# Performance work log

Measured on AMD Instinct MI355X. Metric: run time of the kernel, lower is better.

Reference implementation:

```python
import jax, jax.numpy as jnp
import numpy as np

D_MODEL = 1024
N_HEADS = 16
D_K = D_MODEL // N_HEADS
B, S = 2, 2048


def setup_inputs() -> dict:
    key = jax.random.key(0)
    ks = jax.random.split(key, 5)
    sc = 1.0 / np.sqrt(D_MODEL)
    return {
        "x": jax.random.normal(ks[0], (B, S, D_MODEL), dtype=jnp.float32),
        "W_qkv": jax.random.normal(ks[1], (D_MODEL, 3 * D_MODEL), dtype=jnp.float32) * sc,
        "b_qkv": jnp.zeros((3 * D_MODEL,), dtype=jnp.float32),
        "W_out": jax.random.normal(ks[2], (D_MODEL, D_MODEL), dtype=jnp.float32) * sc,
        "b_out": jnp.zeros((D_MODEL,), dtype=jnp.float32),
    }


def reference(x, W_qkv, b_qkv, W_out, b_out):
    Bb, Ss, _ = x.shape
    qkv = x @ W_qkv + b_qkv                     # [B,S,3*D]
    qkv = qkv.reshape(Bb, Ss, 3, N_HEADS, D_K)
    qkv = jnp.transpose(qkv, (2, 0, 3, 1, 4))   # [3,B,H,S,Dk]
    q, k, v = qkv[0], qkv[1], qkv[2]
    scale = jnp.asarray(np.sqrt(D_K), dtype=x.dtype)
    attn = jnp.einsum('bhsd,bhtd->bhst', q, k) / scale  # [B,H,S,S]
    attn = jax.nn.softmax(attn, axis=-1)
    out = jnp.einsum('bhst,bhtd->bhsd', attn, v)        # [B,H,S,Dk]
    out = jnp.transpose(out, (0, 2, 1, 3)).reshape(Bb, Ss, D_MODEL)
    return out @ W_out + b_out
```

## Files before the change

### kernel.cpp

```cpp
#include <hip/hip_runtime.h>

typedef __bf16 bf16x8 __attribute__((ext_vector_type(8)));
typedef __bf16 bf16x4 __attribute__((ext_vector_type(4)));
typedef float f32x4 __attribute__((ext_vector_type(4)));
typedef unsigned short u16;
typedef unsigned int u32;

__device__ __forceinline__ u16 f2bu(float f) {
  __bf16 h = (__bf16)f;
  return __builtin_bit_cast(u16, h);
}

__device__ __forceinline__ void gld16(const u16* g, const __bf16* lds) {
  __builtin_amdgcn_global_load_lds(
      (const __attribute__((address_space(1))) u32*)(uintptr_t)g,
      (__attribute__((address_space(3))) u32*)(u32)(uintptr_t)lds, 16, 0, 0);
}

__device__ __forceinline__ void tr_tile(const float* __restrict__ in, u16* __restrict__ out,
                                        int R, int C, int bx, int by, int tid) {
  __shared__ u16 t[64][65];
  int tx = tid & 63, ty = tid >> 6;
  int r0 = by * 64, c0 = bx * 64;
  for (int i = 0; i < 16; ++i)
    t[ty + i * 4][tx] = f2bu(in[(size_t)(r0 + ty + i * 4) * C + c0 + tx]);
  __syncthreads();
  for (int i = 0; i < 16; ++i)
    out[(size_t)(c0 + ty + i * 4) * R + r0 + tx] = t[tx][ty + i * 4];
}

__global__ __launch_bounds__(256) void prep(const float* __restrict__ Wqkv,
                                            u16* __restrict__ Wqkv_t,
                                            const float* __restrict__ Wout,
                                            u16* __restrict__ Wout_t,
                                            const float* __restrict__ x,
                                            u16* __restrict__ xb) {
  int id = blockIdx.x, tid = threadIdx.x;
  if (id < 768) {
    tr_tile(Wqkv, Wqkv_t, 1024, 3072, id % 48, id / 48, tid);
  } else if (id < 1024) {
    int id2 = id - 768;
    tr_tile(Wout, Wout_t, 1024, 1024, id2 % 16, id2 / 16, tid);
  } else {
    size_t i = ((size_t)(id - 1024) * 256 + tid) * 8;
    f32x4 a0 = *(const f32x4*)(x + i);
    f32x4 a1 = *(const f32x4*)(x + i + 4);
    bf16x8 v;
    for (int j = 0; j < 4; ++j) { v[j] = (__bf16)a0[j]; v[j + 4] = (__bf16)a1[j]; }
    *(bf16x8*)(xb + i) = v;
  }
}

__global__ __launch_bounds__(256) void transpose_v(const u16* __restrict__ V,
                                                   u16* __restrict__ Vt) {
  constexpr int S = 2048;
  __shared__ u16 t[64][65];
  int bh = blockIdx.y, s0 = blockIdx.x * 64;
  const u16* in = V + (size_t)bh * S * 64;
  u16* out = Vt + (size_t)bh * 64 * S;
  int tx = threadIdx.x & 63, ty = threadIdx.x >> 6;
  for (int i = 0; i < 16; ++i)
    t[ty + i * 4][tx] = in[(size_t)(s0 + ty + i * 4) * 64 + tx];
  __syncthreads();
  for (int i = 0; i < 16; ++i)
    out[(size_t)(ty + i * 4) * S + s0 + tx] = t[tx][ty + i * 4];
}

template <int MODE, int TM, int TN, int MT, int NT, int XM, int XN>
__global__ __launch_bounds__(256) void gemm_bt(const u16* __restrict__ A,
                                               const u16* __restrict__ Bt,
                                               const float* __restrict__ bias,
                                               void* __restrict__ O0v,
                                               u16* __restrict__ O1,
                                               u16* __restrict__ O2,
                                               int M, int N, int K) {
  constexpr int NI = TM / 32;
  constexpr int NJ = TN / 32;
  constexpr int AE = TM * 32;
  constexpr int BE = TN * 32;
  __shared__ __bf16 smem[2 * (AE + BE)];

  int tid = threadIdx.x;
  int w = tid >> 6, lane = tid & 63, quad = lane >> 4, l16 = lane & 15;
  int wr = w >> 1, wc = w & 1;

  int id = blockIdx.x;
  int xcd = id & 7, s0i = id >> 3;
  int mg = xcd % (MT / XM), ng = xcd / (MT / XM);
  int sm = s0i % XM, sn = s0i / XM;
  int m0 = (mg * XM + sm) * TM, n0 = (ng * XN + sn) * TN;

  int srow = w * 16 + (lane >> 2);
  int sch = (lane & 3) ^ ((lane >> 3) & 3);
  const u16* Ag = A + (size_t)(m0 + srow) * K + sch * 8;
  const u16* Bg = Bt + (size_t)(n0 + srow) * K + sch * 8;

  int swl = (quad ^ ((l16 >> 1) & 3)) << 3;

  f32x4 acc[NI][NJ] = {};

#define GLD_STEP(c, kk)                                                          \
  {                                                                              \
    for (int p = 0; p < TM / 64; ++p)                                            \
      gld16(Ag + (size_t)p * 64 * K + (kk), smem + (c) * (AE + BE) + w * 512 + p * 2048); \
    for (int p = 0; p < TN / 64; ++p)                                            \
      gld16(Bg + (size_t)p * 64 * K + (kk), smem + (c) * (AE + BE) + AE + w * 512 + p * 2048); \
  }

  GLD_STEP(0, 0);
  int NS = K / 32;
  for (int s = 0; s < NS; ++s) {
    int cur = s & 1;
    __syncthreads();
    if (s + 1 < NS) GLD_STEP(1 - cur, (s + 1) * 32);
    const __bf16* Asub = smem + cur * (AE + BE);
    const __bf16* Bsub = Asub + AE;
    bf16x8 af[NI], bfr[NJ];
    for (int i = 0; i < NI; ++i)
      af[i] = *(const bf16x8*)(Asub + (wr * (TM / 2) + i * 16 + l16) * 32 + swl);
    for (int j = 0; j < NJ; ++j)
      bfr[j] = *(const bf16x8*)(Bsub + (wc * (TN / 2) + j * 16 + l16) * 32 + swl);
    for (int i = 0; i < NI; ++i)
      for (int j = 0; j < NJ; ++j)
        acc[i][j] = __builtin_amdgcn_mfma_f32_16x16x32_bf16(af[i], bfr[j], acc[i][j], 0, 0, 0);
  }
#undef GLD_STEP

  if (MODE == 0) {
    float* O0 = (float*)O0v;
    for (int j = 0; j < NJ; ++j) {
      int n = n0 + wc * (TN / 2) + j * 16 + l16;
      float bv = bias[n];
      for (int i = 0; i < NI; ++i) {
        int mb = m0 + wr * (TM / 2) + i * 16 + quad * 4;
        for (int r = 0; r < 4; ++r)
          O0[(size_t)(mb + r) * N + n] = acc[i][j][r] + bv;
      }
    }
  } else {
    u16* O0 = (u16*)O0v;
    for (int j = 0; j < NJ; ++j) {
      int n = n0 + wc * (TN / 2) + j * 16 + l16;
      int which = n >> 10, rem = n & 1023, h = rem >> 6, d = rem & 63;
      float bv = bias[n];
      for (int i = 0; i < NI; ++i) {
        for (int r = 0; r < 4; ++r) {
          int m = m0 + wr * (TM / 2) + i * 16 + quad * 4 + r;
          int b = m >> 11, s = m & 2047;
          size_t o = (((size_t)(b * 16 + h)) * 2048 + s) * 64 + d;
          u16 val = f2bu(acc[i][j][r] + bv);
          if (which == 0) O0[o] = val;
          else if (which == 1) O1[o] = val;
          else O2[o] = val;
        }
      }
    }
  }
}

__global__ __launch_bounds__(256, 2) void flash_attn(const u16* __restrict__ Q,
                                                     const u16* __restrict__ K,
                                                     const u16* __restrict__ Vt,
                                                     u16* __restrict__ AO) {
  constexpr int S = 2048;
  __shared__ __bf16 Ks[2][64 * 64];
  __shared__ __bf16 Vs[2][64 * 64];
  __shared__ __bf16 Ps[4][32 * 64];

  int bh = blockIdx.x, qbase = blockIdx.y * 128;
  int tid = threadIdx.x, w = tid >> 6, lane = tid & 63, quad = lane >> 4, l16 = lane & 15;

  const u16* Qh = Q + (size_t)bh * S * 64;
  const u16* Kh = K + (size_t)bh * S * 64;
  const u16* Vh = Vt + (size_t)bh * 64 * S;

  int qrowA = qbase + w * 32 + l16;
  int qrowB = qrowA + 16;
  bf16x8 qf0a = *(const bf16x8*)(Qh + (size_t)qrowA * 64 + quad * 8);
  bf16x8 qf1a = *(const bf16x8*)(Qh + (size_t)qrowA * 64 + 32 + quad * 8);
  bf16x8 qf0b = *(const bf16x8*)(Qh + (size_t)qrowB * 64 + quad * 8);
  bf16x8 qf1b = *(const bf16x8*)(Qh + (size_t)qrowB * 64 + 32 + quad * 8);

  int r0s = tid >> 3, b0s = tid & 7;
  int r1s = r0s + 32;
  int ko0 = r0s * 64 + ((b0s ^ (r0s & 7)) << 3);
  int ko1 = r1s * 64 + ((b0s ^ (r1s & 7)) << 3);

  bf16x8 kr0, kr1, vr0, vr1;
#define LOAD_TILE(tb)                                                   \
  {                                                                     \
    kr0 = *(const bf16x8*)(Kh + (size_t)((tb) + r0s) * 64 + b0s * 8);   \
    kr1 = *(const bf16x8*)(Kh + (size_t)((tb) + r1s) * 64 + b0s * 8);   \
    vr0 = *(const bf16x8*)(Vh + (size_t)r0s * S + (tb) + b0s * 8);      \
    vr1 = *(const bf16x8*)(Vh + (size_t)r1s * S + (tb) + b0s * 8);      \
  }
#define STORE_TILE(c)                                                   \
  {                                                                     \
    *(bf16x8*)(&Ks[c][ko0]) = kr0;                                      \
    *(bf16x8*)(&Ks[c][ko1]) = kr1;                                      \
    *(bf16x8*)(&Vs[c][ko0]) = vr0;                                      \
    *(bf16x8*)(&Vs[c][ko1]) = vr1;                                      \
  }

  LOAD_TILE(0);
  STORE_TILE(0);
  LOAD_TILE(64);
  __syncthreads();

  constexpr float C1 = 0.125f * 1.44269504f;
  constexpr float C0 = -12.0f * 1.44269504f;

  float lA = 0.f, lB = 0.f;
  f32x4 oA[4] = {};
  f32x4 oB[4] = {};
  int xr = l16 & 7;
  int pw_baseA = l16 * 64 + (quad & 1) * 4;
  int pw_baseB = (l16 + 16) * 64 + (quad & 1) * 4;
  int pw_blk = quad >> 1;

  for (int it = 0; it < S / 64; ++it) {
    int c = it & 1;
    if (it + 1 < S / 64) STORE_TILE(1 - c);
    if (it + 2 < S / 64) LOAD_TILE((it + 2) * 64);

    for (int nt = 0; nt < 4; ++nt) {
      const __bf16* kb = &Ks[c][(nt * 16 + l16) * 64];
      bf16x8 kf0 = *(const bf16x8*)(kb + ((quad ^ xr) << 3));
      bf16x8 kf1 = *(const bf16x8*)(kb + (((quad + 4) ^ xr) << 3));
      f32x4 ca = {0.f, 0.f, 0.f, 0.f};
      f32x4 cb = {0.f, 0.f, 0.f, 0.f};
      ca = __builtin_amdgcn_mfma_f32_16x16x32_bf16(kf0, qf0a, ca, 0, 0, 0);
      cb = __builtin_amdgcn_mfma_f32_16x16x32_bf16(kf0, qf0b, cb, 0, 0, 0);
      ca = __builtin_amdgcn_mfma_f32_16x16x32_bf16(kf1, qf1a, ca, 0, 0, 0);
      cb = __builtin_amdgcn_mfma_f32_16x16x32_bf16(kf1, qf1b, cb, 0, 0, 0);
      bf16x4 pka, pkb;
      for (int r = 0; r < 4; ++r) {
        float pa = __builtin_amdgcn_exp2f(fmaf(ca[r], C1, C0));
        float pb = __builtin_amdgcn_exp2f(fmaf(cb[r], C1, C0));
        lA += pa;
        lB += pb;
        pka[r] = (__bf16)pa;
        pkb[r] = (__bf16)pb;
      }
      int pc = (((nt * 2 + pw_blk) ^ xr) << 3);
      *(bf16x4*)(&Ps[w][pw_baseA + pc]) = pka;
      *(bf16x4*)(&Ps[w][pw_baseB + pc]) = pkb;
    }

    bf16x8 pf0a = *(const bf16x8*)(&Ps[w][l16 * 64 + ((quad ^ xr) << 3)]);
    bf16x8 pf1a = *(const bf16x8*)(&Ps[w][l16 * 64 + (((quad + 4) ^ xr) << 3)]);
    bf16x8 pf0b = *(const bf16x8*)(&Ps[w][(l16 + 16) * 64 + ((quad ^ xr) << 3)]);
    bf16x8 pf1b = *(const bf16x8*)(&Ps[w][(l16 + 16) * 64 + (((quad + 4) ^ xr) << 3)]);
    for (int dt = 0; dt < 4; ++dt) {
      const __bf16* vb = &Vs[c][(dt * 16 + l16) * 64];
      bf16x8 v0 = *(const bf16x8*)(vb + ((quad ^ xr) << 3));
      bf16x8 v1 = *(const bf16x8*)(vb + (((quad + 4) ^ xr) << 3));
      oA[dt] = __builtin_amdgcn_mfma_f32_16x16x32_bf16(pf0a, v0, oA[dt], 0, 0, 0);
      oB[dt] = __builtin_amdgcn_mfma_f32_16x16x32_bf16(pf0b, v0, oB[dt], 0, 0, 0);
      oA[dt] = __builtin_amdgcn_mfma_f32_16x16x32_bf16(pf1a, v1, oA[dt], 0, 0, 0);
      oB[dt] = __builtin_amdgcn_mfma_f32_16x16x32_bf16(pf1b, v1, oB[dt], 0, 0, 0);
    }
    __syncthreads();
  }
#undef LOAD_TILE
#undef STORE_TILE

  lA += __shfl_xor(lA, 16);
  lA += __shfl_xor(lA, 32);
  lB += __shfl_xor(lB, 16);
  lB += __shfl_xor(lB, 32);
  float linvA[4], linvB[4];
  for (int r = 0; r < 4; ++r) {
    linvA[r] = 1.f / __shfl(lA, quad * 4 + r);
    linvB[r] = 1.f / __shfl(lB, quad * 4 + r);
  }

  int b = bh >> 4, h = bh & 15;
  for (int dt = 0; dt < 4; ++dt)
    for (int r = 0; r < 4; ++r) {
      int sA = qbase + w * 32 + quad * 4 + r;
      int sB = sA + 16;
      int d = dt * 16 + l16;
      AO[(((size_t)b * 2048 + sA) * 16 + h) * 64 + d] = f2bu(oA[dt][r] * linvA[r]);
      AO[(((size_t)b * 2048 + sB) * 16 + h) * 64 + d] = f2bu(oB[dt][r] * linvB[r]);
    }
}

extern "C" void kernel_launch(void* const* d_in, const int* in_sizes, int n_in,
                              void* d_out, int out_size, void* d_ws, size_t ws_size,
                              hipStream_t stream) {
  const float* x    = (const float*)d_in[0];
  const float* Wqkv = (const float*)d_in[1];
  const float* bqkv = (const float*)d_in[2];
  const float* Wout = (const float*)d_in[3];
  const float* bout = (const float*)d_in[4];
  float* out = (float*)d_out;

  u16* ws = (u16*)d_ws;
  size_t off = 0;
  u16* Wqkv_t = ws + off; off += (size_t)3072 * 1024;
  u16* Wout_t = ws + off; off += (size_t)1024 * 1024;
  u16* xb     = ws + off; off += (size_t)4096 * 1024;
  u16* Qb     = ws + off; off += (size_t)32 * 2048 * 64;
  u16* Kb     = ws + off; off += (size_t)32 * 2048 * 64;
  u16* Vb     = ws + off; off += (size_t)32 * 2048 * 64;
  u16* Vtb    = ws + off; off += (size_t)32 * 2048 * 64;
  u16* AO     = xb;

  prep<<<dim3(3072), 256, 0, stream>>>(Wqkv, Wqkv_t, Wout, Wout_t, x, xb);
  gemm_bt<1, 128, 128, 32, 24, 8, 12><<<dim3(768), 256, 0, stream>>>(
      xb, Wqkv_t, bqkv, (void*)Qb, Kb, Vb, 4096, 3072, 1024);
  transpose_v<<<dim3(32, 32), 256, 0, stream>>>(Vb, Vtb);
  flash_attn<<<dim3(32, 16), 256, 0, stream>>>(Qb, Kb, Vtb, AO);
  gemm_bt<0, 128, 64, 32, 16, 8, 8><<<dim3(512), 256, 0, stream>>>(
      AO, Wout_t, bout, (void*)out, nullptr, nullptr, 4096, 1024, 1024);
}
```

Before: 180.0 us.

## Fuse V transpose into QKV GEMM epilogue and load K/V directly into registers

The QKV GEMM epilogue now writes V already transposed, using vectorized 4-element stores, so the separate transpose kernel and its V buffer are gone. Flash attention drops LDS staging and __syncthreads for K and V. Each lane loads its MFMA fragments straight from global memory, with K prefetched one tile ahead in registers. The grid is remapped so heads are grouped per XCD for L2 locality, and MFMA sections get raised wave priority. The trade-off is more register pressure and redundant global loads across waves in exchange for removing LDS traffic, barriers and one kernel launch.

```diff
diff --git a/kernel.cpp b/kernel.cpp
--- a/kernel.cpp
+++ b/kernel.cpp
@@ -4,6 +4,7 @@
 typedef __bf16 bf16x4 __attribute__((ext_vector_type(4)));
 typedef float f32x4 __attribute__((ext_vector_type(4)));
 typedef unsigned short u16;
+typedef unsigned short u16x4 __attribute__((ext_vector_type(4)));
 typedef unsigned int u32;
 
 __device__ __forceinline__ u16 f2bu(float f) {
@@ -51,21 +52,6 @@
   }
 }
 
-__global__ __launch_bounds__(256) void transpose_v(const u16* __restrict__ V,
-                                                   u16* __restrict__ Vt) {
-  constexpr int S = 2048;
-  __shared__ u16 t[64][65];
-  int bh = blockIdx.y, s0 = blockIdx.x * 64;
-  const u16* in = V + (size_t)bh * S * 64;
-  u16* out = Vt + (size_t)bh * 64 * S;
-  int tx = threadIdx.x & 63, ty = threadIdx.x >> 6;
-  for (int i = 0; i < 16; ++i)
-    t[ty + i * 4][tx] = in[(size_t)(s0 + ty + i * 4) * 64 + tx];
-  __syncthreads();
-  for (int i = 0; i < 16; ++i)
-    out[(size_t)(ty + i * 4) * S + s0 + tx] = t[tx][ty + i * 4];
-}
-
 template <int MODE, int TM, int TN, int MT, int NT, int XM, int XN>
 __global__ __launch_bounds__(256) void gemm_bt(const u16* __restrict__ A,
                                                const u16* __restrict__ Bt,
@@ -144,14 +130,16 @@
       int which = n >> 10, rem = n & 1023, h = rem >> 6, d = rem & 63;
       float bv = bias[n];
       for (int i = 0; i < NI; ++i) {
-        for (int r = 0; r < 4; ++r) {
-          int m = m0 + wr * (TM / 2) + i * 16 + quad * 4 + r;
-          int b = m >> 11, s = m & 2047;
-          size_t o = (((size_t)(b * 16 + h)) * 2048 + s) * 64 + d;
-          u16 val = f2bu(acc[i][j][r] + bv);
-          if (which == 0) O0[o] = val;
-          else if (which == 1) O1[o] = val;
-          else O2[o] = val;
+        int m = m0 + wr * (TM / 2) + i * 16 + quad * 4;
+        int b = m >> 11, s = m & 2047;
+        if (which == 2) {
+          u16x4 val;
+          for (int r = 0; r < 4; ++r) val[r] = f2bu(acc[i][j][r] + bv);
+          *(u16x4*)(O2 + (((size_t)(b * 16 + h)) * 64 + d) * 2048 + s) = val;
+        } else {
+          u16* Od = which ? O1 : O0;
+          for (int r = 0; r < 4; ++r)
+            Od[(((size_t)(b * 16 + h)) * 2048 + (s + r)) * 64 + d] = f2bu(acc[i][j][r] + bv);
         }
       }
     }
@@ -163,11 +151,14 @@
                                                      const u16* __restrict__ Vt,
                                                      u16* __restrict__ AO) {
   constexpr int S = 2048;
-  __shared__ __bf16 Ks[2][64 * 64];
-  __shared__ __bf16 Vs[2][64 * 64];
+  constexpr int NITER = S / 64;
   __shared__ __bf16 Ps[4][32 * 64];
 
-  int bh = blockIdx.x, qbase = blockIdx.y * 128;
+  int id = blockIdx.x;
+  int xcd = id & 7, kk = id >> 3;
+  int bh = xcd * 4 + (kk & 3);
+  int qbase = (kk >> 2) * 128;
+
   int tid = threadIdx.x, w = tid >> 6, lane = tid & 63, quad = lane >> 4, l16 = lane & 15;
 
   const u16* Qh = Q + (size_t)bh * S * 64;
@@ -181,31 +172,8 @@
   bf16x8 qf0b = *(const bf16x8*)(Qh + (size_t)qrowB * 64 + quad * 8);
   bf16x8 qf1b = *(const bf16x8*)(Qh + (size_t)qrowB * 64 + 32 + quad * 8);
 
-  int r0s = tid >> 3, b0s = tid & 7;
-  int r1s = r0s + 32;
-  int ko0 = r0s * 64 + ((b0s ^ (r0s & 7)) << 3);
-  int ko1 = r1s * 64 + ((b0s ^ (r1s & 7)) << 3);
-
-  bf16x8 kr0, kr1, vr0, vr1;
-#define LOAD_TILE(tb)                                                   \
-  {                                                                     \
-    kr0 = *(const bf16x8*)(Kh + (size_t)((tb) + r0s) * 64 + b0s * 8);   \
-    kr1 = *(const bf16x8*)(Kh + (size_t)((tb) + r1s) * 64 + b0s * 8);   \
-    vr0 = *(const bf16x8*)(Vh + (size_t)r0s * S + (tb) + b0s * 8);      \
-    vr1 = *(const bf16x8*)(Vh + (size_t)r1s * S + (tb) + b0s * 8);      \
-  }
-#define STORE_TILE(c)                                                   \
-  {                                                                     \
-    *(bf16x8*)(&Ks[c][ko0]) = kr0;                                      \
-    *(bf16x8*)(&Ks[c][ko1]) = kr1;                                      \
-    *(bf16x8*)(&Vs[c][ko0]) = vr0;                                      \
-    *(bf16x8*)(&Vs[c][ko1]) = vr1;                                      \
-  }
-
-  LOAD_TILE(0);
-  STORE_TILE(0);
-  LOAD_TILE(64);
-  __syncthreads();
+  const u16* Kp = Kh + (size_t)l16 * 64 + quad * 8;
+  const u16* Vp = Vh + (size_t)l16 * S + quad * 8;
 
   constexpr float C1 = 0.125f * 1.44269504f;
   constexpr float C0 = -12.0f * 1.44269504f;
@@ -218,22 +186,42 @@
   int pw_baseB = (l16 + 16) * 64 + (quad & 1) * 4;
   int pw_blk = quad >> 1;
 
-  for (int it = 0; it < S / 64; ++it) {
-    int c = it & 1;
-    if (it + 1 < S / 64) STORE_TILE(1 - c);
-    if (it + 2 < S / 64) LOAD_TILE((it + 2) * 64);
-
+  bf16x8 kf[8];
+#pragma unroll
+  for (int nt = 0; nt < 4; ++nt) {
+    kf[2 * nt]     = *(const bf16x8*)(Kp + (size_t)(nt * 16) * 64);
+    kf[2 * nt + 1] = *(const bf16x8*)(Kp + (size_t)(nt * 16) * 64 + 32);
+  }
+
+#pragma unroll 2
+  for (int it = 0; it < NITER; ++it) {
+    int tb = it * 64;
+    bf16x8 vv[8];
+#pragma unroll
+    for (int dt = 0; dt < 4; ++dt) {
+      vv[2 * dt]     = *(const bf16x8*)(Vp + (size_t)(dt * 16) * S + tb);
+      vv[2 * dt + 1] = *(const bf16x8*)(Vp + (size_t)(dt * 16) * S + tb + 32);
+    }
+    int nb = (it + 1 < NITER) ? tb + 64 : tb;
+    bf16x8 kn[8];
+#pragma unroll
     for (int nt = 0; nt < 4; ++nt) {
-      const __bf16* kb = &Ks[c][(nt * 16 + l16) * 64];
-      bf16x8 kf0 = *(const bf16x8*)(kb + ((quad ^ xr) << 3));
-      bf16x8 kf1 = *(const bf16x8*)(kb + (((quad + 4) ^ xr) << 3));
+      kn[2 * nt]     = *(const bf16x8*)(Kp + (size_t)(nb + nt * 16) * 64);
+      kn[2 * nt + 1] = *(const bf16x8*)(Kp + (size_t)(nb + nt * 16) * 64 + 32);
+    }
+
+#pragma unroll
+    for (int nt = 0; nt < 4; ++nt) {
       f32x4 ca = {0.f, 0.f, 0.f, 0.f};
       f32x4 cb = {0.f, 0.f, 0.f, 0.f};
-      ca = __builtin_amdgcn_mfma_f32_16x16x32_bf16(kf0, qf0a, ca, 0, 0, 0);
-      cb = __builtin_amdgcn_mfma_f32_16x16x32_bf16(kf0, qf0b, cb, 0, 0, 0);
-      ca = __builtin_amdgcn_mfma_f32_16x16x32_bf16(kf1, qf1a, ca, 0, 0, 0);
-      cb = __builtin_amdgcn_mfma_f32_16x16x32_bf16(kf1, qf1b, cb, 0, 0, 0);
+      __builtin_amdgcn_s_setprio(1);
+      ca = __builtin_amdgcn_mfma_f32_16x16x32_bf16(kf[2 * nt], qf0a, ca, 0, 0, 0);
+      cb = __builtin_amdgcn_mfma_f32_16x16x32_bf16(kf[2 * nt], qf0b, cb, 0, 0, 0);
+      ca = __builtin_amdgcn_mfma_f32_16x16x32_bf16(kf[2 * nt + 1], qf1a, ca, 0, 0, 0);
+      cb = __builtin_amdgcn_mfma_f32_16x16x32_bf16(kf[2 * nt + 1], qf1b, cb, 0, 0, 0);
+      __builtin_amdgcn_s_setprio(0);
       bf16x4 pka, pkb;
+#pragma unroll
       for (int r = 0; r < 4; ++r) {
         float pa = __builtin_amdgcn_exp2f(fmaf(ca[r], C1, C0));
         float pb = __builtin_amdgcn_exp2f(fmaf(cb[r], C1, C0));
@@ -251,19 +239,19 @@
     bf16x8 pf1a = *(const bf16x8*)(&Ps[w][l16 * 64 + (((quad + 4) ^ xr) << 3)]);
     bf16x8 pf0b = *(const bf16x8*)(&Ps[w][(l16 + 16) * 64 + ((quad ^ xr) << 3)]);
     bf16x8 pf1b = *(const bf16x8*)(&Ps[w][(l16 + 16) * 64 + (((quad + 4) ^ xr) << 3)]);
+#pragma unroll
     for (int dt = 0; dt < 4; ++dt) {
-      const __bf16* vb = &Vs[c][(dt * 16 + l16) * 64];
-      bf16x8 v0 = *(const bf16x8*)(vb + ((quad ^ xr) << 3));
-      bf16x8 v1 = *(const bf16x8*)(vb + (((quad + 4) ^ xr) << 3));
-      oA[dt] = __builtin_amdgcn_mfma_f32_16x16x32_bf16(pf0a, v0, oA[dt], 0, 0, 0);
-      oB[dt] = __builtin_amdgcn_mfma_f32_16x16x32_bf16(pf0b, v0, oB[dt], 0, 0, 0);
-      oA[dt] = __builtin_amdgcn_mfma_f32_16x16x32_bf16(pf1a, v1, oA[dt], 0, 0, 0);
-      oB[dt] = __builtin_amdgcn_mfma_f32_16x16x32_bf16(pf1b, v1, oB[dt], 0, 0, 0);
-    }
-    __syncthreads();
-  }
-#undef LOAD_TILE
-#undef STORE_TILE
+      __builtin_amdgcn_s_setprio(1);
+      oA[dt] = __builtin_amdgcn_mfma_f32_16x16x32_bf16(pf0a, vv[2 * dt], oA[dt], 0, 0, 0);
+      oB[dt] = __builtin_amdgcn_mfma_f32_16x16x32_bf16(pf0b, vv[2 * dt], oB[dt], 0, 0, 0);
+      oA[dt] = __builtin_amdgcn_mfma_f32_16x16x32_bf16(pf1a, vv[2 * dt + 1], oA[dt], 0, 0, 0);
+      oB[dt] = __builtin_amdgcn_mfma_f32_16x16x32_bf16(pf1b, vv[2 * dt + 1], oB[dt], 0, 0, 0);
+      __builtin_amdgcn_s_setprio(0);
+    }
+
+#pragma unroll
+    for (int z = 0; z < 8; ++z) kf[z] = kn[z];
+  }
 
   lA += __shfl_xor(lA, 16);
   lA += __shfl_xor(lA, 32);
@@ -303,15 +291,13 @@
   u16* xb     = ws + off; off += (size_t)4096 * 1024;
   u16* Qb     = ws + off; off += (size_t)32 * 2048 * 64;
   u16* Kb     = ws + off; off += (size_t)32 * 2048 * 64;
-  u16* Vb     = ws + off; off += (size_t)32 * 2048 * 64;
   u16* Vtb    = ws + off; off += (size_t)32 * 2048 * 64;
   u16* AO     = xb;
 
   prep<<<dim3(3072), 256, 0, stream>>>(Wqkv, Wqkv_t, Wout, Wout_t, x, xb);
   gemm_bt<1, 128, 128, 32, 24, 8, 12><<<dim3(768), 256, 0, stream>>>(
-      xb, Wqkv_t, bqkv, (void*)Qb, Kb, Vb, 4096, 3072, 1024);
-  transpose_v<<<dim3(32, 32), 256, 0, stream>>>(Vb, Vtb);
-  flash_attn<<<dim3(32, 16), 256, 0, stream>>>(Qb, Kb, Vtb, AO);
+      xb, Wqkv_t, bqkv, (void*)Qb, Kb, Vtb, 4096, 3072, 1024);
+  flash_attn<<<dim3(512), 256, 0, stream>>>(Qb, Kb, Vtb, AO);
   gemm_bt<0, 128, 64, 32, 16, 8, 8><<<dim3(512), 256, 0, stream>>>(
       AO, Wout_t, bout, (void*)out, nullptr, nullptr, 4096, 1024, 1024);
 }
```

Result: slower. 247.6 us (+37.5%).
